# Optimization experiments

Hardware: AMD Instinct MI355X
Metric: run time of the kernel (lower is better)

## Reference

```python
import jax, jax.numpy as jnp
import numpy as np

EMB = 1024
HID = 1024
VOCAB = 50257


def _lstm_cell(x, h, c, Wih, Whh, bih, bhh):
    # PyTorch gate order: i, f, g, o
    gates = x @ Wih.T + bih + h @ Whh.T + bhh  # [1, 4H]
    i, f, g, o = jnp.split(gates, 4, axis=-1)
    c_new = jax.nn.sigmoid(f) * c + jax.nn.sigmoid(i) * jnp.tanh(g)
    h_new = jax.nn.sigmoid(o) * jnp.tanh(c_new)
    return h_new, c_new


def setup_inputs() -> dict:
    key = jax.random.key(0)
    ks = jax.random.split(key, 16)
    s = 0.02
    return {
        "word_input": jax.random.randint(ks[0], (1,), 0, VOCAB),
        "h0": jax.random.normal(ks[1], (2, 1, HID), jnp.float32),
        "c0": jax.random.normal(ks[2], (2, 1, HID), jnp.float32),
        "emb": jax.random.normal(ks[3], (VOCAB, EMB), jnp.float32) * s,
        "W_ih0": jax.random.normal(ks[4], (4 * HID, EMB), jnp.float32) * s,
        "W_hh0": jax.random.normal(ks[5], (4 * HID, HID), jnp.float32) * s,
        "b_ih0": jax.random.normal(ks[6], (4 * HID,), jnp.float32) * s,
        "b_hh0": jax.random.normal(ks[7], (4 * HID,), jnp.float32) * s,
        "W_ih1": jax.random.normal(ks[8], (4 * HID, HID), jnp.float32) * s,
        "W_hh1": jax.random.normal(ks[9], (4 * HID, HID), jnp.float32) * s,
        "b_ih1": jax.random.normal(ks[10], (4 * HID,), jnp.float32) * s,
        "b_hh1": jax.random.normal(ks[11], (4 * HID,), jnp.float32) * s,
        "W_out": jax.random.normal(ks[12], (VOCAB, HID), jnp.float32) * s,
        "b_out": jax.random.normal(ks[13], (VOCAB,), jnp.float32) * s,
    }


def reference(word_input, h0, c0, emb, W_ih0, W_hh0, b_ih0, b_hh0,
              W_ih1, W_hh1, b_ih1, b_hh1, W_out, b_out):
    # embedding lookup + ReLU, batch=1 seq=1
    x = jax.nn.relu(emb[word_input])                 # [1, EMB]
    # 2-layer LSTM single step (dropout disabled / eval mode)
    h1, c1 = _lstm_cell(x, h0[0], c0[0], W_ih0, W_hh0, b_ih0, b_hh0)
    h2, c2 = _lstm_cell(h1, h0[1], c0[1], W_ih1, W_hh1, b_ih1, b_hh1)
    logits = h2 @ W_out.T + b_out                    # [1, VOCAB]
    log_probas = jax.nn.log_softmax(logits, axis=1)
    h_out = jnp.stack([h1, h2])                      # [2, 1, HID]
    c_out = jnp.stack([c1, c2])
    return log_probas, (h_out, c_out)
```

## Files before the change

kernel.cpp:

```cpp
#include <hip/hip_runtime.h>
#include <math.h>

#define EMB 1024
#define HID 1024
#define VOCAB 50257
#define HOUT_OFF VOCAB
#define COUT_OFF (VOCAB + 2*HID)
#define ROWS_PER_BLOCK 16
#define NB_LOGITS ((VOCAB + ROWS_PER_BLOCK - 1) / ROWS_PER_BLOCK)

__device__ __forceinline__ float wave_reduce(float v) {
#pragma unroll
    for (int o = 32; o > 0; o >>= 1) v += __shfl_down(v, o);
    return v;
}

__device__ __forceinline__ float sigmoidf_(float x) { return 1.0f / (1.0f + expf(-x)); }

__global__ __launch_bounds__(256) void lstm_gemv(
    const float* __restrict__ Wih, const float* __restrict__ Whh,
    const float* __restrict__ bih, const float* __restrict__ bhh,
    const float* __restrict__ emb, const int* __restrict__ word,
    const float* __restrict__ x_in,
    const float* __restrict__ h_prev, const float* __restrict__ c_prev,
    float* __restrict__ h_ws, float* __restrict__ out, int layer)
{
    const int r    = blockIdx.x;
    const int wave = threadIdx.x >> 6;
    const int lane = threadIdx.x & 63;
    const int row  = wave * HID + r;

    float4 xv[4], hv[4];
    if (x_in != nullptr) {
#pragma unroll
        for (int j = 0; j < 4; ++j) xv[j] = ((const float4*)x_in)[j*64 + lane];
    } else {
        const float4* e = (const float4*)(emb + (size_t)word[0] * EMB);
#pragma unroll
        for (int j = 0; j < 4; ++j) {
            float4 v = e[j*64 + lane];
            v.x = fmaxf(v.x, 0.f); v.y = fmaxf(v.y, 0.f);
            v.z = fmaxf(v.z, 0.f); v.w = fmaxf(v.w, 0.f);
            xv[j] = v;
        }
    }
#pragma unroll
    for (int j = 0; j < 4; ++j) hv[j] = ((const float4*)h_prev)[j*64 + lane];

    const float4* wih = (const float4*)(Wih + (size_t)row * EMB);
    const float4* whh = (const float4*)(Whh + (size_t)row * HID);
    float acc = 0.f;
#pragma unroll
    for (int j = 0; j < 4; ++j) {
        float4 a = wih[j*64 + lane];
        acc += a.x*xv[j].x + a.y*xv[j].y + a.z*xv[j].z + a.w*xv[j].w;
        float4 b = whh[j*64 + lane];
        acc += b.x*hv[j].x + b.y*hv[j].y + b.z*hv[j].z + b.w*hv[j].w;
    }
    acc = wave_reduce(acc);

    __shared__ float gates[4];
    if (lane == 0) gates[wave] = acc + bih[row] + bhh[row];
    __syncthreads();

    if (threadIdx.x == 0) {
        float ig = sigmoidf_(gates[0]);
        float fg = sigmoidf_(gates[1]);
        float gg = tanhf(gates[2]);
        float og = sigmoidf_(gates[3]);
        float c  = fg * c_prev[r] + ig * gg;
        float h  = og * tanhf(c);
        h_ws[r] = h;
        out[HOUT_OFF + layer * HID + r] = h;
        out[COUT_OFF + layer * HID + r] = c;
    }
}

__global__ __launch_bounds__(256) void logits_gemv(
    const float* __restrict__ W, const float* __restrict__ b,
    const float* __restrict__ x, float* __restrict__ out,
    float* __restrict__ partials)
{
    const int wave = threadIdx.x >> 6;
    const int lane = threadIdx.x & 63;

    float4 xv[4];
#pragma unroll
    for (int j = 0; j < 4; ++j) xv[j] = ((const float4*)x)[j*64 + lane];

    float m = -INFINITY, s = 0.f;
    const int base = blockIdx.x * ROWS_PER_BLOCK + wave * 4;
#pragma unroll
    for (int k = 0; k < 4; ++k) {
        int row = base + k;
        if (row >= VOCAB) break;
        const float4* wr = (const float4*)(W + (size_t)row * HID);
        float acc = 0.f;
#pragma unroll
        for (int j = 0; j < 4; ++j) {
            float4 a = wr[j*64 + lane];
            acc += a.x*xv[j].x + a.y*xv[j].y + a.z*xv[j].z + a.w*xv[j].w;
        }
        acc = wave_reduce(acc);
        if (lane == 0) {
            float logit = acc + b[row];
            out[row] = logit;
            float nm = fmaxf(m, logit);
            s = s * expf(m - nm) + expf(logit - nm);
            m = nm;
        }
    }

    __shared__ float ms[4], ss[4];
    if (lane == 0) { ms[wave] = m; ss[wave] = s; }
    __syncthreads();
    if (threadIdx.x == 0) {
        float M = ms[0], S = ss[0];
#pragma unroll
        for (int w = 1; w < 4; ++w) {
            float nm = fmaxf(M, ms[w]);
            S = S * expf(M - nm) + ss[w] * expf(ms[w] - nm);
            M = nm;
        }
        partials[2 * blockIdx.x]     = M;
        partials[2 * blockIdx.x + 1] = S;
    }
}

__global__ __launch_bounds__(256) void softmax_combine(
    const float* __restrict__ partials, int nb, float* __restrict__ s_out)
{
    float M = -INFINITY, S = 0.f;
    for (int p = threadIdx.x; p < nb; p += 256) {
        float m = partials[2*p], s = partials[2*p + 1];
        float nm = fmaxf(M, m);
        S = S * expf(M - nm) + s * expf(m - nm);
        M = nm;
    }
    __shared__ float ms[256], ss[256];
    ms[threadIdx.x] = M; ss[threadIdx.x] = S;
    __syncthreads();
    for (int o = 128; o > 0; o >>= 1) {
        if (threadIdx.x < (unsigned)o) {
            float m2 = ms[threadIdx.x + o], s2 = ss[threadIdx.x + o];
            float m1 = ms[threadIdx.x];
            float nm = fmaxf(m1, m2);
            ss[threadIdx.x] = ss[threadIdx.x] * expf(m1 - nm) + s2 * expf(m2 - nm);
            ms[threadIdx.x] = nm;
        }
        __syncthreads();
    }
    if (threadIdx.x == 0) s_out[0] = ms[0] + logf(ss[0]);
}

__global__ __launch_bounds__(256) void logsoftmax_sub(
    float* __restrict__ out, const float* __restrict__ s_ptr, int n)
{
    int i = blockIdx.x * 256 + threadIdx.x;
    if (i < n) out[i] -= s_ptr[0];
}

extern "C" void kernel_launch(void* const* d_in, const int* in_sizes, int n_in,
                              void* d_out, int out_size, void* d_ws, size_t ws_size,
                              hipStream_t stream)
{
    const int*   word = (const int*)  d_in[0];
    const float* h0   = (const float*)d_in[1];
    const float* c0   = (const float*)d_in[2];
    const float* emb  = (const float*)d_in[3];
    const float* Wih0 = (const float*)d_in[4];
    const float* Whh0 = (const float*)d_in[5];
    const float* bih0 = (const float*)d_in[6];
    const float* bhh0 = (const float*)d_in[7];
    const float* Wih1 = (const float*)d_in[8];
    const float* Whh1 = (const float*)d_in[9];
    const float* bih1 = (const float*)d_in[10];
    const float* bhh1 = (const float*)d_in[11];
    const float* Wout = (const float*)d_in[12];
    const float* bout = (const float*)d_in[13];

    float* out = (float*)d_out;
    float* ws  = (float*)d_ws;
    float* h1       = ws;
    float* h2       = ws + HID;
    float* partials = ws + 2 * HID;
    float* s_ptr    = ws + 2 * HID + 2 * NB_LOGITS;

    lstm_gemv<<<HID, 256, 0, stream>>>(Wih0, Whh0, bih0, bhh0, emb, word,
                                       nullptr, h0, c0, h1, out, 0);
    lstm_gemv<<<HID, 256, 0, stream>>>(Wih1, Whh1, bih1, bhh1, emb, word,
                                       h1, h0 + HID, c0 + HID, h2, out, 1);
    logits_gemv<<<NB_LOGITS, 256, 0, stream>>>(Wout, bout, h2, out, partials);
    softmax_combine<<<1, 256, 0, stream>>>(partials, NB_LOGITS, s_ptr);
    logsoftmax_sub<<<(VOCAB + 255) / 256, 256, 0, stream>>>(out, s_ptr, VOCAB);
}
```

Before: 439.0 us.

## Fuse LSTM layers, logits GEMV and log-softmax into one persistent kernel

Replaces the five separate launches (two LSTM GEMVs, logits GEMV, softmax combine, subtract) with one persistent kernel of 1024 blocks. The stages are separated by a hand-rolled atomic grid barrier on a counter that is zeroed with a memset before launch. Each block now loops over vocabulary tiles for the logits, and the log-sum-exp combine is done redundantly in every block before each block subtracts its slice. The aim is to remove per-launch overhead and the tail gaps between kernels. The barrier relies on all 1024 blocks being co-resident, which a normal launch does not guarantee, so a deadlock is possible.

```diff
diff --git a/kernel.cpp b/kernel.cpp
--- a/kernel.cpp
+++ b/kernel.cpp
@@ -8,6 +8,7 @@
 #define COUT_OFF (VOCAB + 2*HID)
 #define ROWS_PER_BLOCK 16
 #define NB_LOGITS ((VOCAB + ROWS_PER_BLOCK - 1) / ROWS_PER_BLOCK)
+#define GRID_BLKS 1024
 
 __device__ __forceinline__ float wave_reduce(float v) {
 #pragma unroll
@@ -17,35 +18,43 @@
 
 __device__ __forceinline__ float sigmoidf_(float x) { return 1.0f / (1.0f + expf(-x)); }
 
-__global__ __launch_bounds__(256) void lstm_gemv(
+__device__ __forceinline__ void grid_sync(unsigned* bar, unsigned target) {
+    __threadfence();
+    __syncthreads();
+    if (threadIdx.x == 0) {
+        __hip_atomic_fetch_add(bar, 1u, __ATOMIC_ACQ_REL, __HIP_MEMORY_SCOPE_AGENT);
+        unsigned v;
+        do {
+            __builtin_amdgcn_s_sleep(1);
+            v = __hip_atomic_load(bar, __ATOMIC_ACQUIRE, __HIP_MEMORY_SCOPE_AGENT);
+        } while (v < target);
+    }
+    __syncthreads();
+    __threadfence();
+}
+
+__device__ __forceinline__ void lstm_layer(
     const float* __restrict__ Wih, const float* __restrict__ Whh,
     const float* __restrict__ bih, const float* __restrict__ bhh,
-    const float* __restrict__ emb, const int* __restrict__ word,
-    const float* __restrict__ x_in,
+    const float* __restrict__ x, bool relu_x,
     const float* __restrict__ h_prev, const float* __restrict__ c_prev,
-    float* __restrict__ h_ws, float* __restrict__ out, int layer)
+    float* __restrict__ h_ws, float* __restrict__ out, int layer, int r)
 {
-    const int r    = blockIdx.x;
     const int wave = threadIdx.x >> 6;
     const int lane = threadIdx.x & 63;
     const int row  = wave * HID + r;
 
     float4 xv[4], hv[4];
-    if (x_in != nullptr) {
-#pragma unroll
-        for (int j = 0; j < 4; ++j) xv[j] = ((const float4*)x_in)[j*64 + lane];
-    } else {
-        const float4* e = (const float4*)(emb + (size_t)word[0] * EMB);
-#pragma unroll
-        for (int j = 0; j < 4; ++j) {
-            float4 v = e[j*64 + lane];
+#pragma unroll
+    for (int j = 0; j < 4; ++j) {
+        float4 v = ((const float4*)x)[j*64 + lane];
+        if (relu_x) {
             v.x = fmaxf(v.x, 0.f); v.y = fmaxf(v.y, 0.f);
             v.z = fmaxf(v.z, 0.f); v.w = fmaxf(v.w, 0.f);
-            xv[j] = v;
-        }
-    }
-#pragma unroll
-    for (int j = 0; j < 4; ++j) hv[j] = ((const float4*)h_prev)[j*64 + lane];
+        }
+        xv[j] = v;
+        hv[j] = ((const float4*)h_prev)[j*64 + lane];
+    }
 
     const float4* wih = (const float4*)(Wih + (size_t)row * EMB);
     const float4* whh = (const float4*)(Whh + (size_t)row * HID);
@@ -74,40 +83,64 @@
         out[HOUT_OFF + layer * HID + r] = h;
         out[COUT_OFF + layer * HID + r] = c;
     }
-}
-
-__global__ __launch_bounds__(256) void logits_gemv(
-    const float* __restrict__ W, const float* __restrict__ b,
-    const float* __restrict__ x, float* __restrict__ out,
-    float* __restrict__ partials)
+    __syncthreads();
+}
+
+__global__ __launch_bounds__(256, 4) void fused_decoder(
+    const float* __restrict__ Wih0, const float* __restrict__ Whh0,
+    const float* __restrict__ bih0, const float* __restrict__ bhh0,
+    const float* __restrict__ Wih1, const float* __restrict__ Whh1,
+    const float* __restrict__ bih1, const float* __restrict__ bhh1,
+    const float* __restrict__ emb,  const int* __restrict__ word,
+    const float* __restrict__ h0,   const float* __restrict__ c0,
+    const float* __restrict__ Wout, const float* __restrict__ bout,
+    float* __restrict__ out, float* __restrict__ ws)
 {
+    const int b = blockIdx.x;
+    unsigned* bar   = (unsigned*)ws;
+    float* h1       = ws + 16;
+    float* h2       = ws + 16 + HID;
+    float* partials = ws + 16 + 2*HID;
+
+    lstm_layer(Wih0, Whh0, bih0, bhh0,
+               emb + (size_t)word[0] * EMB, true,
+               h0, c0, h1, out, 0, b);
+    grid_sync(bar, 1u * GRID_BLKS);
+
+    lstm_layer(Wih1, Whh1, bih1, bhh1,
+               h1, false,
+               h0 + HID, c0 + HID, h2, out, 1, b);
+    grid_sync(bar, 2u * GRID_BLKS);
+
     const int wave = threadIdx.x >> 6;
     const int lane = threadIdx.x & 63;
 
     float4 xv[4];
 #pragma unroll
-    for (int j = 0; j < 4; ++j) xv[j] = ((const float4*)x)[j*64 + lane];
+    for (int j = 0; j < 4; ++j) xv[j] = ((const float4*)h2)[j*64 + lane];
 
     float m = -INFINITY, s = 0.f;
-    const int base = blockIdx.x * ROWS_PER_BLOCK + wave * 4;
-#pragma unroll
-    for (int k = 0; k < 4; ++k) {
-        int row = base + k;
-        if (row >= VOCAB) break;
-        const float4* wr = (const float4*)(W + (size_t)row * HID);
-        float acc = 0.f;
-#pragma unroll
-        for (int j = 0; j < 4; ++j) {
-            float4 a = wr[j*64 + lane];
-            acc += a.x*xv[j].x + a.y*xv[j].y + a.z*xv[j].z + a.w*xv[j].w;
-        }
-        acc = wave_reduce(acc);
-        if (lane == 0) {
-            float logit = acc + b[row];
-            out[row] = logit;
-            float nm = fmaxf(m, logit);
-            s = s * expf(m - nm) + expf(logit - nm);
-            m = nm;
+    for (int tile = b; tile < NB_LOGITS; tile += GRID_BLKS) {
+        const int base = tile * ROWS_PER_BLOCK + wave * 4;
+#pragma unroll
+        for (int k = 0; k < 4; ++k) {
+            const int row = base + k;
+            const int rc  = row < VOCAB ? row : VOCAB - 1;
+            const float4* wr = (const float4*)(Wout + (size_t)rc * HID);
+            float acc = 0.f;
+#pragma unroll
+            for (int j = 0; j < 4; ++j) {
+                float4 a = wr[j*64 + lane];
+                acc += a.x*xv[j].x + a.y*xv[j].y + a.z*xv[j].z + a.w*xv[j].w;
+            }
+            acc = wave_reduce(acc);
+            if (lane == 0 && row < VOCAB) {
+                float logit = acc + bout[row];
+                out[row] = logit;
+                float nm = fmaxf(m, logit);
+                s = s * expf(m - nm) + expf(logit - nm);
+                m = nm;
+            }
         }
     }
 
@@ -122,42 +155,35 @@
             S = S * expf(M - nm) + ss[w] * expf(ms[w] - nm);
             M = nm;
         }
-        partials[2 * blockIdx.x]     = M;
-        partials[2 * blockIdx.x + 1] = S;
-    }
-}
-
-__global__ __launch_bounds__(256) void softmax_combine(
-    const float* __restrict__ partials, int nb, float* __restrict__ s_out)
-{
+        partials[2*b]     = M;
+        partials[2*b + 1] = S;
+    }
+    grid_sync(bar, 3u * GRID_BLKS);
+
     float M = -INFINITY, S = 0.f;
-    for (int p = threadIdx.x; p < nb; p += 256) {
-        float m = partials[2*p], s = partials[2*p + 1];
-        float nm = fmaxf(M, m);
-        S = S * expf(M - nm) + s * expf(m - nm);
+    for (int p = threadIdx.x; p < GRID_BLKS; p += 256) {
+        float mm = partials[2*p], sp = partials[2*p + 1];
+        float nm = fmaxf(M, mm);
+        S = S * expf(M - nm) + sp * expf(mm - nm);
         M = nm;
     }
-    __shared__ float ms[256], ss[256];
-    ms[threadIdx.x] = M; ss[threadIdx.x] = S;
+    __shared__ float msr[256], ssr[256];
+    msr[threadIdx.x] = M; ssr[threadIdx.x] = S;
     __syncthreads();
     for (int o = 128; o > 0; o >>= 1) {
         if (threadIdx.x < (unsigned)o) {
-            float m2 = ms[threadIdx.x + o], s2 = ss[threadIdx.x + o];
-            float m1 = ms[threadIdx.x];
+            float m2 = msr[threadIdx.x + o], s2 = ssr[threadIdx.x + o];
+            float m1 = msr[threadIdx.x];
             float nm = fmaxf(m1, m2);
-            ss[threadIdx.x] = ss[threadIdx.x] * expf(m1 - nm) + s2 * expf(m2 - nm);
-            ms[threadIdx.x] = nm;
+            ssr[threadIdx.x] = ssr[threadIdx.x] * expf(m1 - nm) + s2 * expf(m2 - nm);
+            msr[threadIdx.x] = nm;
         }
         __syncthreads();
     }
-    if (threadIdx.x == 0) s_out[0] = ms[0] + logf(ss[0]);
-}
-
-__global__ __launch_bounds__(256) void logsoftmax_sub(
-    float* __restrict__ out, const float* __restrict__ s_ptr, int n)
-{
-    int i = blockIdx.x * 256 + threadIdx.x;
-    if (i < n) out[i] -= s_ptr[0];
+    const float lse = msr[0] + logf(ssr[0]);
+
+    const int idx = b * 256 + (int)threadIdx.x;
+    if (idx < VOCAB) out[idx] -= lse;
 }
 
 extern "C" void kernel_launch(void* const* d_in, const int* in_sizes, int n_in,
@@ -181,16 +207,12 @@
 
     float* out = (float*)d_out;
     float* ws  = (float*)d_ws;
-    float* h1       = ws;
-    float* h2       = ws + HID;
-    float* partials = ws + 2 * HID;
-    float* s_ptr    = ws + 2 * HID + 2 * NB_LOGITS;
-
-    lstm_gemv<<<HID, 256, 0, stream>>>(Wih0, Whh0, bih0, bhh0, emb, word,
-                                       nullptr, h0, c0, h1, out, 0);
-    lstm_gemv<<<HID, 256, 0, stream>>>(Wih1, Whh1, bih1, bhh1, emb, word,
-                                       h1, h0 + HID, c0 + HID, h2, out, 1);
-    logits_gemv<<<NB_LOGITS, 256, 0, stream>>>(Wout, bout, h2, out, partials);
-    softmax_combine<<<1, 256, 0, stream>>>(partials, NB_LOGITS, s_ptr);
-    logsoftmax_sub<<<(VOCAB + 255) / 256, 256, 0, stream>>>(out, s_ptr, VOCAB);
-}
+
+    hipMemsetAsync(ws, 0, 64, stream);
+
+    hipLaunchKernelGGL(fused_decoder, dim3(GRID_BLKS), dim3(256), 0, stream,
+                       Wih0, Whh0, bih0, bhh0,
+                       Wih1, Whh1, bih1, bhh1,
+                       emb, word, h0, c0,
+                       Wout, bout, out, ws);
+}
```

Result: slower. 1.227 ms (+179.4%).
